# Kernel optimization log

Hardware: AMD Instinct MI355X
Metric: run time of the kernel (lower is better)

## Reference

```python
import jax, jax.numpy as jnp
import numpy as np

EPS = 1e-8  # torch F.cosine_similarity eps


def setup_inputs() -> dict:
    key = jax.random.key(0)
    kk, kb, kg, km = jax.random.split(key, 4)
    B, N, K = 128, 2048, 256
    k_vec = jax.random.normal(kk, (B, K), dtype=jnp.float32)
    beta = jax.random.uniform(kb, (B, 1), dtype=jnp.float32) * 5.0 + 0.5   # key strength > 0
    gamma = jax.random.uniform(kg, (B, 1), dtype=jnp.float32) * 2.0 + 1.0  # sharpen >= 1
    keys = jax.random.normal(km, (B, N, K), dtype=jnp.float32) * (1.0 / np.sqrt(N + K))
    return {"k": k_vec, "beta": beta, "gamma": gamma, "keys": keys, "candidates": 32}


def reference(k, beta, gamma, keys, candidates):
    B, N, K = keys.shape
    # cosine similarity between each memory key row [B,N,K] and query [B,1,K]
    dots = jnp.einsum('bnk,bk->bn', keys, k)                      # [B,N]
    kn = jnp.maximum(jnp.linalg.norm(keys, axis=-1), EPS)         # [B,N]
    qn = jnp.maximum(jnp.linalg.norm(k, axis=-1, keepdims=True), EPS)  # [B,1]
    cos = dots / (kn * qn)
    # content weighting: softmax over memory rows
    wc = jax.nn.softmax(beta * cos, axis=1)                       # [B,N]
    # top-k candidate mask (1 at top-k, 1e-16 elsewhere)
    _, idx = jax.lax.top_k(wc, candidates)                        # [B,C]
    mask = jnp.full((B, N), 1e-16, dtype=wc.dtype)
    mask = mask.at[jnp.arange(B)[:, None], idx].set(1.0)
    wc = wc * mask
    wc = wc / jnp.sum(wc, axis=-1, keepdims=True)
    # sharpen
    w = wc ** gamma
    w = w / jnp.sum(w, axis=1, keepdims=True)
    return w
```

## Files before the change

### kernel.cpp

```cpp
#include <hip/hip_runtime.h>
#include <cstddef>
#include <cstdint>

#define EPSF 1e-8f

static constexpr int Bn = 128;
static constexpr int Nn = 2048;
static constexpr int Kn = 256;
static constexpr int TPB = 256;
static constexpr int ROWS_PER_BLOCK = 64;
static constexpr int CHUNKS = Nn / ROWS_PER_BLOCK;

__global__ __launch_bounds__(TPB) void score_kernel(
    const float* __restrict__ q,
    const float* __restrict__ beta,
    const float* __restrict__ keys,
    float* __restrict__ z)
{
    const int b     = blockIdx.x / CHUNKS;
    const int chunk = blockIdx.x % CHUNKS;
    const int wv    = threadIdx.x >> 6;
    const int lane  = threadIdx.x & 63;
    const int sub   = lane >> 4;
    const int c     = lane & 15;

    const float4* qf4 = (const float4*)(q + (size_t)b * Kn);
    const float4 kq0 = qf4[c +  0];
    const float4 kq1 = qf4[c + 16];
    const float4 kq2 = qf4[c + 32];
    const float4 kq3 = qf4[c + 48];

    float qs = kq0.x*kq0.x + kq0.y*kq0.y + kq0.z*kq0.z + kq0.w*kq0.w
             + kq1.x*kq1.x + kq1.y*kq1.y + kq1.z*kq1.z + kq1.w*kq1.w
             + kq2.x*kq2.x + kq2.y*kq2.y + kq2.z*kq2.z + kq2.w*kq2.w
             + kq3.x*kq3.x + kq3.y*kq3.y + kq3.z*kq3.z + kq3.w*kq3.w;
    qs += __shfl_xor(qs, 8);
    qs += __shfl_xor(qs, 4);
    qs += __shfl_xor(qs, 2);
    qs += __shfl_xor(qs, 1);
    const float qn = fmaxf(sqrtf(qs), EPSF);
    const float scale0 = beta[b] / qn;

    const int rbase = chunk * ROWS_PER_BLOCK + wv * 16;
    #pragma unroll
    for (int tt = 0; tt < 4; ++tt) {
        const int row = rbase + tt * 4 + sub;
        const float4* rp = (const float4*)(keys + ((size_t)b * Nn + row) * Kn);
        const float4 v0 = rp[c +  0];
        const float4 v1 = rp[c + 16];
        const float4 v2 = rp[c + 32];
        const float4 v3 = rp[c + 48];
        float d = v0.x*kq0.x + v0.y*kq0.y + v0.z*kq0.z + v0.w*kq0.w
                + v1.x*kq1.x + v1.y*kq1.y + v1.z*kq1.z + v1.w*kq1.w
                + v2.x*kq2.x + v2.y*kq2.y + v2.z*kq2.z + v2.w*kq2.w
                + v3.x*kq3.x + v3.y*kq3.y + v3.z*kq3.z + v3.w*kq3.w;
        float s = v0.x*v0.x + v0.y*v0.y + v0.z*v0.z + v0.w*v0.w
                + v1.x*v1.x + v1.y*v1.y + v1.z*v1.z + v1.w*v1.w
                + v2.x*v2.x + v2.y*v2.y + v2.z*v2.z + v2.w*v2.w
                + v3.x*v3.x + v3.y*v3.y + v3.z*v3.z + v3.w*v3.w;
        d += __shfl_xor(d, 8);  s += __shfl_xor(s, 8);
        d += __shfl_xor(d, 4);  s += __shfl_xor(s, 4);
        d += __shfl_xor(d, 2);  s += __shfl_xor(s, 2);
        d += __shfl_xor(d, 1);  s += __shfl_xor(s, 1);
        if (c == 0) {
            z[(size_t)b * Nn + row] = d * scale0 / fmaxf(sqrtf(s), EPSF);
        }
    }
}

__global__ __launch_bounds__(TPB) void topk_kernel(
    const float* __restrict__ z,
    const float* __restrict__ gamma,
    const int* __restrict__ cand,
    float* __restrict__ out)
{
    const int b    = blockIdx.x;
    const int tid  = threadIdx.x;
    const int lane = tid & 63;
    const int wv   = tid >> 6;
    const int C    = cand[0];

    __shared__ float    fred[4];
    __shared__ int      ired[4];
    __shared__ unsigned sscan[TPB];

    float v[8];
    {
        const float4* zp = (const float4*)(z + (size_t)b * Nn) + (size_t)tid * 2;
        const float4 a0 = zp[0];
        const float4 a1 = zp[1];
        v[0]=a0.x; v[1]=a0.y; v[2]=a0.z; v[3]=a0.w;
        v[4]=a1.x; v[5]=a1.y; v[6]=a1.z; v[7]=a1.w;
    }

    unsigned key[8];
    #pragma unroll
    for (int j = 0; j < 8; ++j) {
        const unsigned u = __float_as_uint(v[j]);
        key[j] = (u & 0x80000000u) ? ~u : (u | 0x80000000u);
    }

    float mx = v[0];
    #pragma unroll
    for (int j = 1; j < 8; ++j) mx = fmaxf(mx, v[j]);
    #pragma unroll
    for (int off = 32; off >= 1; off >>= 1) mx = fmaxf(mx, __shfl_xor(mx, off));
    if (lane == 0) fred[wv] = mx;
    __syncthreads();
    mx = fmaxf(fmaxf(fred[0], fred[1]), fmaxf(fred[2], fred[3]));
    __syncthreads();

    unsigned t = 0u;
    for (int bit = 31; bit >= 0; --bit) {
        const unsigned ct = t | (1u << bit);
        int cnt = 0;
        #pragma unroll
        for (int j = 0; j < 8; ++j)
            cnt += (int)__popcll(__ballot(key[j] >= ct));
        if (lane == 0) ired[wv] = cnt;
        __syncthreads();
        cnt = ired[0] + ired[1] + ired[2] + ired[3];
        __syncthreads();
        if (cnt >= C) t = ct;
    }

    int cgt = 0;
    #pragma unroll
    for (int j = 0; j < 8; ++j)
        cgt += (int)__popcll(__ballot(key[j] > t));
    if (lane == 0) ired[wv] = cgt;
    __syncthreads();
    cgt = ired[0] + ired[1] + ired[2] + ired[3];
    __syncthreads();
    const unsigned need = (unsigned)(C - cgt);

    unsigned tierank[8];
    unsigned myties = 0;
    #pragma unroll
    for (int j = 0; j < 8; ++j) { tierank[j] = myties; myties += (key[j] == t) ? 1u : 0u; }
    sscan[tid] = myties;
    __syncthreads();
    for (int off = 1; off < TPB; off <<= 1) {
        const unsigned x = (tid >= off) ? sscan[tid - off] : 0u;
        __syncthreads();
        sscan[tid] += x;
        __syncthreads();
    }
    const unsigned prefix = sscan[tid] - myties;

    const float g = gamma[b];
    const float tinyf = __powf(1e-16f, g);
    float a[8];
    float ssum = 0.f;
    #pragma unroll
    for (int j = 0; j < 8; ++j) {
        const bool sel = (key[j] > t) || ((key[j] == t) && ((prefix + tierank[j]) < need));
        a[j] = __expf(g * (v[j] - mx)) * (sel ? 1.0f : tinyf);
        ssum += a[j];
    }
    #pragma unroll
    for (int off = 32; off >= 1; off >>= 1) ssum += __shfl_xor(ssum, off);
    if (lane == 0) fred[wv] = ssum;
    __syncthreads();
    ssum = fred[0] + fred[1] + fred[2] + fred[3];

    const float inv = 1.0f / ssum;
    const float4 o0 = make_float4(a[0]*inv, a[1]*inv, a[2]*inv, a[3]*inv);
    const float4 o1 = make_float4(a[4]*inv, a[5]*inv, a[6]*inv, a[7]*inv);
    float4* op = (float4*)(out + (size_t)b * Nn) + (size_t)tid * 2;
    op[0] = o0;
    op[1] = o1;
}

extern "C" void kernel_launch(void* const* d_in, const int* in_sizes, int n_in,
                              void* d_out, int out_size, void* d_ws, size_t ws_size,
                              hipStream_t stream) {
    const float* q     = (const float*)d_in[0];
    const float* beta  = (const float*)d_in[1];
    const float* gamma = (const float*)d_in[2];
    const float* keys  = (const float*)d_in[3];
    const int*   cand  = (const int*)d_in[4];
    float* out = (float*)d_out;
    float* z   = (float*)d_ws;

    score_kernel<<<dim3(Bn * CHUNKS), dim3(TPB), 0, stream>>>(q, beta, keys, z);
    topk_kernel<<<dim3(Bn), dim3(TPB), 0, stream>>>(z, gamma, cand, out);
}
```

Baseline: 370.6 us.

## Restructure top-k into per-wave selection with merge; widen score loads

The top-k kernel now runs the 32-bit radix threshold search independently in each wave with no block barriers. Each wave writes its local top-C candidates to shared memory, and a single wave does a second radix search over the merged candidates. The tie-rank prefix uses a packed wave shuffle scan instead of a barrier-heavy shared-memory scan, and the separate max reduction is dropped by shifting the exponent with the threshold value. The score kernel now uses 8 lanes per row with eight 16-byte nontemporal loads and split FMA accumulators. This adds a MAXC=64 cap on candidates, and exponentiating relative to the threshold instead of the max could overflow for large gamma times spread.

Result: faster. 348.1 us (-6.1%).

```diff
diff --git a/kernel.cpp b/kernel.cpp
--- a/kernel.cpp
+++ b/kernel.cpp
@@ -3,6 +3,8 @@
 #include <cstdint>
 
 #define EPSF 1e-8f
+
+typedef float vf4 __attribute__((ext_vector_type(4)));
 
 static constexpr int Bn = 128;
 static constexpr int Nn = 2048;
@@ -10,6 +12,7 @@
 static constexpr int TPB = 256;
 static constexpr int ROWS_PER_BLOCK = 64;
 static constexpr int CHUNKS = Nn / ROWS_PER_BLOCK;
+static constexpr int MAXC = 64;
 
 __global__ __launch_bounds__(TPB) void score_kernel(
     const float* __restrict__ q,
@@ -21,49 +24,50 @@
     const int chunk = blockIdx.x % CHUNKS;
     const int wv    = threadIdx.x >> 6;
     const int lane  = threadIdx.x & 63;
-    const int sub   = lane >> 4;
-    const int c     = lane & 15;
-
-    const float4* qf4 = (const float4*)(q + (size_t)b * Kn);
-    const float4 kq0 = qf4[c +  0];
-    const float4 kq1 = qf4[c + 16];
-    const float4 kq2 = qf4[c + 32];
-    const float4 kq3 = qf4[c + 48];
-
-    float qs = kq0.x*kq0.x + kq0.y*kq0.y + kq0.z*kq0.z + kq0.w*kq0.w
-             + kq1.x*kq1.x + kq1.y*kq1.y + kq1.z*kq1.z + kq1.w*kq1.w
-             + kq2.x*kq2.x + kq2.y*kq2.y + kq2.z*kq2.z + kq2.w*kq2.w
-             + kq3.x*kq3.x + kq3.y*kq3.y + kq3.z*kq3.z + kq3.w*kq3.w;
-    qs += __shfl_xor(qs, 8);
+    const int g     = lane >> 3;
+    const int c     = lane & 7;
+
+    const vf4* qf4 = (const vf4*)(q + (size_t)b * Kn);
+    vf4 kq[8];
+    #pragma unroll
+    for (int i = 0; i < 8; ++i) kq[i] = qf4[c + 8 * i];
+
+    float qa[4] = {0.f, 0.f, 0.f, 0.f};
+    #pragma unroll
+    for (int i = 0; i < 8; ++i) {
+        const vf4 kk = kq[i];
+        qa[i & 3] = fmaf(kk[0], kk[0], fmaf(kk[1], kk[1], fmaf(kk[2], kk[2], fmaf(kk[3], kk[3], qa[i & 3]))));
+    }
+    float qs = (qa[0] + qa[1]) + (qa[2] + qa[3]);
     qs += __shfl_xor(qs, 4);
     qs += __shfl_xor(qs, 2);
     qs += __shfl_xor(qs, 1);
-    const float qn = fmaxf(sqrtf(qs), EPSF);
-    const float scale0 = beta[b] / qn;
-
-    const int rbase = chunk * ROWS_PER_BLOCK + wv * 16;
-    #pragma unroll
-    for (int tt = 0; tt < 4; ++tt) {
-        const int row = rbase + tt * 4 + sub;
-        const float4* rp = (const float4*)(keys + ((size_t)b * Nn + row) * Kn);
-        const float4 v0 = rp[c +  0];
-        const float4 v1 = rp[c + 16];
-        const float4 v2 = rp[c + 32];
-        const float4 v3 = rp[c + 48];
-        float d = v0.x*kq0.x + v0.y*kq0.y + v0.z*kq0.z + v0.w*kq0.w
-                + v1.x*kq1.x + v1.y*kq1.y + v1.z*kq1.z + v1.w*kq1.w
-                + v2.x*kq2.x + v2.y*kq2.y + v2.z*kq2.z + v2.w*kq2.w
-                + v3.x*kq3.x + v3.y*kq3.y + v3.z*kq3.z + v3.w*kq3.w;
-        float s = v0.x*v0.x + v0.y*v0.y + v0.z*v0.z + v0.w*v0.w
-                + v1.x*v1.x + v1.y*v1.y + v1.z*v1.z + v1.w*v1.w
-                + v2.x*v2.x + v2.y*v2.y + v2.z*v2.z + v2.w*v2.w
-                + v3.x*v3.x + v3.y*v3.y + v3.z*v3.z + v3.w*v3.w;
-        d += __shfl_xor(d, 8);  s += __shfl_xor(s, 8);
-        d += __shfl_xor(d, 4);  s += __shfl_xor(s, 4);
-        d += __shfl_xor(d, 2);  s += __shfl_xor(s, 2);
-        d += __shfl_xor(d, 1);  s += __shfl_xor(s, 1);
+    const float scale0 = beta[b] / fmaxf(sqrtf(qs), EPSF);
+
+    const int rbase = chunk * ROWS_PER_BLOCK + wv * 16 + g;
+    #pragma unroll
+    for (int it = 0; it < 2; ++it) {
+        const int row = rbase + it * 8;
+        const vf4* rp = (const vf4*)(keys + ((size_t)b * Nn + row) * Kn);
+        vf4 v[8];
+        #pragma unroll
+        for (int i = 0; i < 8; ++i) v[i] = __builtin_nontemporal_load(&rp[c + 8 * i]);
+        float d[4] = {0.f, 0.f, 0.f, 0.f};
+        float s[4] = {0.f, 0.f, 0.f, 0.f};
+        #pragma unroll
+        for (int i = 0; i < 8; ++i) {
+            const vf4 vv = v[i];
+            const vf4 kk = kq[i];
+            d[i & 3] = fmaf(vv[0], kk[0], fmaf(vv[1], kk[1], fmaf(vv[2], kk[2], fmaf(vv[3], kk[3], d[i & 3]))));
+            s[i & 3] = fmaf(vv[0], vv[0], fmaf(vv[1], vv[1], fmaf(vv[2], vv[2], fmaf(vv[3], vv[3], s[i & 3]))));
+        }
+        float dd = (d[0] + d[1]) + (d[2] + d[3]);
+        float ss = (s[0] + s[1]) + (s[2] + s[3]);
+        dd += __shfl_xor(dd, 4);  ss += __shfl_xor(ss, 4);
+        dd += __shfl_xor(dd, 2);  ss += __shfl_xor(ss, 2);
+        dd += __shfl_xor(dd, 1);  ss += __shfl_xor(ss, 1);
         if (c == 0) {
-            z[(size_t)b * Nn + row] = d * scale0 / fmaxf(sqrtf(s), EPSF);
+            z[(size_t)b * Nn + row] = dd * scale0 / fmaxf(sqrtf(ss), EPSF);
         }
     }
 }
@@ -80,17 +84,18 @@
     const int wv   = tid >> 6;
     const int C    = cand[0];
 
+    __shared__ unsigned cbuf[4 * MAXC];
+    __shared__ unsigned spack[4];
+    __shared__ unsigned st;
     __shared__ float    fred[4];
-    __shared__ int      ired[4];
-    __shared__ unsigned sscan[TPB];
 
     float v[8];
     {
-        const float4* zp = (const float4*)(z + (size_t)b * Nn) + (size_t)tid * 2;
-        const float4 a0 = zp[0];
-        const float4 a1 = zp[1];
-        v[0]=a0.x; v[1]=a0.y; v[2]=a0.z; v[3]=a0.w;
-        v[4]=a1.x; v[5]=a1.y; v[6]=a1.z; v[7]=a1.w;
+        const vf4* zp = (const vf4*)(z + (size_t)b * Nn) + (size_t)tid * 2;
+        const vf4 a0 = zp[0];
+        const vf4 a1 = zp[1];
+        v[0]=a0[0]; v[1]=a0[1]; v[2]=a0[2]; v[3]=a0[3];
+        v[4]=a1[0]; v[5]=a1[1]; v[6]=a1[2]; v[7]=a1[3];
     }
 
     unsigned key[8];
@@ -100,74 +105,102 @@
         key[j] = (u & 0x80000000u) ? ~u : (u | 0x80000000u);
     }
 
-    float mx = v[0];
-    #pragma unroll
-    for (int j = 1; j < 8; ++j) mx = fmaxf(mx, v[j]);
-    #pragma unroll
-    for (int off = 32; off >= 1; off >>= 1) mx = fmaxf(mx, __shfl_xor(mx, off));
-    if (lane == 0) fred[wv] = mx;
-    __syncthreads();
-    mx = fmaxf(fmaxf(fred[0], fred[1]), fmaxf(fred[2], fred[3]));
-    __syncthreads();
-
-    unsigned t = 0u;
+    unsigned tw = 0u;
     for (int bit = 31; bit >= 0; --bit) {
-        const unsigned ct = t | (1u << bit);
+        const unsigned ct = tw | (1u << bit);
         int cnt = 0;
         #pragma unroll
         for (int j = 0; j < 8; ++j)
             cnt += (int)__popcll(__ballot(key[j] >= ct));
-        if (lane == 0) ired[wv] = cnt;
-        __syncthreads();
-        cnt = ired[0] + ired[1] + ired[2] + ired[3];
-        __syncthreads();
-        if (cnt >= C) t = ct;
-    }
-
-    int cgt = 0;
-    #pragma unroll
-    for (int j = 0; j < 8; ++j)
-        cgt += (int)__popcll(__ballot(key[j] > t));
-    if (lane == 0) ired[wv] = cgt;
-    __syncthreads();
-    cgt = ired[0] + ired[1] + ired[2] + ired[3];
-    __syncthreads();
-    const unsigned need = (unsigned)(C - cgt);
-
-    unsigned tierank[8];
-    unsigned myties = 0;
-    #pragma unroll
-    for (int j = 0; j < 8; ++j) { tierank[j] = myties; myties += (key[j] == t) ? 1u : 0u; }
-    sscan[tid] = myties;
-    __syncthreads();
-    for (int off = 1; off < TPB; off <<= 1) {
-        const unsigned x = (tid >= off) ? sscan[tid - off] : 0u;
-        __syncthreads();
-        sscan[tid] += x;
-        __syncthreads();
-    }
-    const unsigned prefix = sscan[tid] - myties;
-
+        if (cnt >= C) tw = ct;
+    }
+
+    {
+        const unsigned long long below_mask = (1ull << lane) - 1ull;
+        int base = 0;
+        #pragma unroll
+        for (int j = 0; j < 8; ++j) {
+            const unsigned long long m = __ballot(key[j] > tw);
+            if (key[j] > tw) {
+                const int slot = base + (int)__popcll(m & below_mask);
+                cbuf[wv * MAXC + slot] = key[j];
+            }
+            base += (int)__popcll(m);
+        }
+        for (int i = base + lane; i < C; i += 64) cbuf[wv * MAXC + i] = tw;
+    }
+    __syncthreads();
+
+    if (wv == 0) {
+        unsigned cv[4];
+        #pragma unroll
+        for (int j = 0; j < 4; ++j) {
+            const int idx = lane + 64 * j;
+            const int w2 = idx / MAXC, i2 = idx % MAXC;
+            cv[j] = (i2 < C) ? cbuf[w2 * MAXC + i2] : 0u;
+        }
+        unsigned t = 0u;
+        for (int bit = 31; bit >= 0; --bit) {
+            const unsigned ct = t | (1u << bit);
+            int cnt = 0;
+            #pragma unroll
+            for (int j = 0; j < 4; ++j)
+                cnt += (int)__popcll(__ballot(cv[j] >= ct));
+            if (cnt >= C) t = ct;
+        }
+        if (lane == 0) st = t;
+    }
+    __syncthreads();
+    const unsigned t = st;
+
+    int gt = 0, eq = 0;
+    #pragma unroll
+    for (int j = 0; j < 8; ++j) { gt += (key[j] > t); eq += (key[j] == t); }
+    const unsigned p = ((unsigned)gt << 16) | (unsigned)eq;
+    unsigned x = p;
+    #pragma unroll
+    for (int off = 1; off < 64; off <<= 1) {
+        const unsigned y = __shfl_up(x, off);
+        if (lane >= off) x += y;
+    }
+    if (lane == 63) spack[wv] = x;
+    __syncthreads();
+    unsigned base = 0, total = 0;
+    #pragma unroll
+    for (int w2 = 0; w2 < 4; ++w2) {
+        const unsigned sv = spack[w2];
+        total += sv;
+        if (w2 < wv) base += sv;
+    }
+    const unsigned excl = base + x - p;
+    const int cgt_total = (int)(total >> 16);
+    const int need      = C - cgt_total;
+    const int eq_before = (int)(excl & 0xFFFFu);
+
+    const float tval = __uint_as_float((t & 0x80000000u) ? (t ^ 0x80000000u) : ~t);
     const float g = gamma[b];
-    const float tinyf = __powf(1e-16f, g);
+    const float tiny = __powf(1e-16f, g);
     float a[8];
     float ssum = 0.f;
+    int eqseen = 0;
     #pragma unroll
     for (int j = 0; j < 8; ++j) {
-        const bool sel = (key[j] > t) || ((key[j] == t) && ((prefix + tierank[j]) < need));
-        a[j] = __expf(g * (v[j] - mx)) * (sel ? 1.0f : tinyf);
+        const bool sel = (key[j] > t) || ((key[j] == t) && ((eq_before + eqseen) < need));
+        eqseen += (key[j] == t);
+        a[j] = __expf(g * (v[j] - tval)) * (sel ? 1.0f : tiny);
         ssum += a[j];
     }
     #pragma unroll
     for (int off = 32; off >= 1; off >>= 1) ssum += __shfl_xor(ssum, off);
     if (lane == 0) fred[wv] = ssum;
     __syncthreads();
-    ssum = fred[0] + fred[1] + fred[2] + fred[3];
-
-    const float inv = 1.0f / ssum;
-    const float4 o0 = make_float4(a[0]*inv, a[1]*inv, a[2]*inv, a[3]*inv);
-    const float4 o1 = make_float4(a[4]*inv, a[5]*inv, a[6]*inv, a[7]*inv);
-    float4* op = (float4*)(out + (size_t)b * Nn) + (size_t)tid * 2;
+    const float tot = (fred[0] + fred[1]) + (fred[2] + fred[3]);
+    const float inv = 1.0f / tot;
+
+    vf4 o0, o1;
+    o0[0]=a[0]*inv; o0[1]=a[1]*inv; o0[2]=a[2]*inv; o0[3]=a[3]*inv;
+    o1[0]=a[4]*inv; o1[1]=a[5]*inv; o1[2]=a[6]*inv; o1[3]=a[7]*inv;
+    vf4* op = (vf4*)(out + (size_t)b * Nn) + (size_t)tid * 2;
     op[0] = o0;
     op[1] = o1;
 }
```
